# Kernel optimization log

Measured on AMD Instinct MI355X. Metric: run time of the kernel, lower is better.

## Reference

```python
import jax, jax.numpy as jnp
import numpy as np

N, E = 50000, 800000
D, H, C, ED = 128, 8, 16, 32  # in_channels, heads, head_dim, edge_dim
EPS = 1e-5

def _ln(x, g, b):
    mu = jnp.mean(x, axis=-1, keepdims=True)
    var = jnp.mean((x - mu) ** 2, axis=-1, keepdims=True)
    return (x - mu) * jax.lax.rsqrt(var + EPS) * g + b

def setup_inputs() -> dict:
    key = jax.random.key(0)
    ks = jax.random.split(key, 20)
    s = 0.05
    inp = {
        'x': jax.random.normal(ks[0], (N, D), jnp.float32),
        'edge_index': jax.random.randint(ks[1], (2, E), 0, N, jnp.int64),
        'edge_attr': jax.random.normal(ks[2], (E, ED), jnp.float32),
        'Wq': jax.random.normal(ks[3], (D, H * C)) * s,
        'bq': jnp.zeros((H * C,)),
        'Wk': jax.random.normal(ks[4], (D, H * C)) * s,
        'bk': jnp.zeros((H * C,)),
        'Wv': jax.random.normal(ks[5], (D, H * C)) * s,
        'bv': jnp.zeros((H * C,)),
        'We': jax.random.normal(ks[6], (ED, H * C)) * s,
        'Wskip': jax.random.normal(ks[7], (D, H * C)) * s,
        'bskip': jnp.zeros((H * C,)),
        'ln1_g': jnp.ones((D,)), 'ln1_b': jnp.zeros((D,)),
        'W1': jax.random.normal(ks[8], (D, 4 * D)) * s,
        'b1': jnp.zeros((4 * D,)),
        'W2': jax.random.normal(ks[9], (4 * D, D)) * s,
        'b2': jnp.zeros((D,)),
        'ln2_g': jnp.ones((D,)), 'ln2_b': jnp.zeros((D,)),
    }
    return inp

def reference(x, edge_index, edge_attr, Wq, bq, Wk, bk, Wv, bv, We, Wskip, bskip,
              ln1_g, ln1_b, W1, b1, W2, b2, ln2_g, ln2_b):
    src, dst = edge_index[0], edge_index[1]
    # node-level projections, then gather per-edge  [N,H,C] -> [E,H,C]
    q = (x @ Wq + bq).reshape(N, H, C)
    k = (x @ Wk + bk).reshape(N, H, C)
    v = (x @ Wv + bv).reshape(N, H, C)
    e = (edge_attr @ We).reshape(E, H, C)
    k_e = k[src] + e
    alpha = jnp.sum(q[dst] * k_e, axis=-1) / jnp.sqrt(jnp.float32(C))  # [E,H]
    # segment softmax over destination nodes
    m = jax.ops.segment_max(alpha, dst, num_segments=N)               # [N,H]
    p = jnp.exp(alpha - m[dst])
    denom = jax.ops.segment_sum(p, dst, num_segments=N)
    a = p / (denom[dst] + 1e-16)
    out_e = (v[src] + e) * a[..., None]                               # [E,H,C]
    attn = jax.ops.segment_sum(out_e, dst, num_segments=N).reshape(N, H * C)
    attn = attn + x @ Wskip + bskip  # root/skip connection
    # transformer block: residual + LN + FFN + LN (dropout = identity, eval)
    h = _ln(x + attn, ln1_g, ln1_b)
    ffn = jax.nn.relu(h @ W1 + b1) @ W2 + b2
    return _ln(h + ffn, ln2_g, ln2_b)
```

## Files before the change

kernel.cpp:

```cpp
#include <hip/hip_runtime.h>
#include <hip/hip_bf16.h>

using bf16 = __hip_bfloat16;
typedef __attribute__((ext_vector_type(8))) short short8;
typedef __attribute__((ext_vector_type(4))) float floatx4;

#define NN 50000
#define EE 800000
#define DD 128
#define HH 8
#define CC 16
#define EDD 32
#define DF 512

__device__ __forceinline__ float b2f(bf16 v) { return __bfloat162float(v); }
__device__ __forceinline__ float bs2f(short s) {
    bf16 h = *reinterpret_cast<bf16*>(&s);
    return __bfloat162float(h);
}
__device__ __forceinline__ float bu2f(unsigned short s) {
    unsigned int u = ((unsigned int)s) << 16;
    return *reinterpret_cast<float*>(&u);
}
__device__ __forceinline__ short f2bs(float v) {
    bf16 h = __float2bfloat16(v);
    return *reinterpret_cast<short*>(&h);
}

__global__ void k_detect(const int* __restrict__ ei, int* __restrict__ flag)
{
    if (threadIdx.x == 0 && blockIdx.x == 0) {
        int all0 = 1;
        for (int i = 0; i < 16; ++i) all0 &= (ei[2 * i + 1] == 0);
        flag[0] = all0;
    }
}

__device__ __forceinline__ int load_src(const int* ei, int is64, int i)
{
    int s = is64 ? ei[2 * i] : ei[i];
    return (s < 0) ? 0 : (s >= NN ? NN - 1 : s);
}
__device__ __forceinline__ int load_dst(const int* ei, int is64, int i)
{
    int d = is64 ? ei[2 * EE + 2 * i] : ei[EE + i];
    return (d < 0) ? 0 : (d >= NN ? NN - 1 : d);
}

__global__ void k_packall(const float* __restrict__ Wq, const float* __restrict__ Wk,
                          const float* __restrict__ Wv, const float* __restrict__ Wsk,
                          const float* __restrict__ W1, const float* __restrict__ W2,
                          const float* __restrict__ We,
                          bf16* __restrict__ wqp, bf16* __restrict__ wkp,
                          bf16* __restrict__ wvp, bf16* __restrict__ wskp,
                          bf16* __restrict__ w1p, bf16* __restrict__ w2p,
                          bf16* __restrict__ wep)
{
    int idx = blockIdx.x * 256 + threadIdx.x;
    const float* W; bf16* out; int ksteps, N, local;
    if (idx < 65536) {
        int wsel = idx >> 14; local = idx & 16383;
        W   = (wsel == 0) ? Wq  : (wsel == 1) ? Wk  : (wsel == 2) ? Wv  : Wsk;
        out = (wsel == 0) ? wqp : (wsel == 1) ? wkp : (wsel == 2) ? wvp : wskp;
        ksteps = 4; N = 128;
    } else if (idx < 131072) { local = idx - 65536;  W = W1; out = w1p; ksteps = 4;  N = 512; }
    else if (idx < 196608)   { local = idx - 131072; W = W2; out = w2p; ksteps = 16; N = 128; }
    else if (idx < 200704)   { local = idx - 196608; W = We; out = wep; ksteps = 1;  N = 128; }
    else return;
    int j = local & 7, lane = (local >> 3) & 63, rest = local >> 9;
    int kstep = rest % ksteps, ntile = rest / ksteps;
    int quad = lane >> 4, m = lane & 15;
    int k = kstep * 32 + quad * 8 + j;
    int n = ntile * 16 + m;
    out[local] = __float2bfloat16(W[(size_t)k * N + n]);
}

__global__ __launch_bounds__(256) void k_proj(
    const float* __restrict__ x,
    const bf16* __restrict__ wqp, const bf16* __restrict__ wkp,
    const bf16* __restrict__ wvp, const bf16* __restrict__ wskp,
    const float* __restrict__ bq, const float* __restrict__ bk,
    const float* __restrict__ bv, const float* __restrict__ bsk,
    bf16* __restrict__ qb, bf16* __restrict__ kb, bf16* __restrict__ vb,
    bf16* __restrict__ skipb)
{
    __shared__ __align__(16) short xs[32][136];
    __shared__ __align__(16) short os[32][520];
    const int t = threadIdx.x;
    const int wave = t >> 6, lane = t & 63;
    const int quad = lane >> 4, m = lane & 15;
    const int n0 = blockIdx.x * 32;

    for (int idx = t; idx < 32 * 32; idx += 256) {
        int row = idx >> 5, g = idx & 31;
        int node = n0 + row;
        float4 xv = {0.f, 0.f, 0.f, 0.f};
        if (node < NN) xv = *reinterpret_cast<const float4*>(&x[(size_t)node * 128 + g * 4]);
        short4 s4;
        s4.x = f2bs(xv.x); s4.y = f2bs(xv.y); s4.z = f2bs(xv.z); s4.w = f2bs(xv.w);
        *reinterpret_cast<short4*>(&xs[row][g * 4]) = s4;
    }
    __syncthreads();

    const bf16* Wp = (wave == 0) ? wqp : (wave == 1) ? wkp : (wave == 2) ? wvp : wskp;
    const float* bias = (wave == 0) ? bq : (wave == 1) ? bk : (wave == 2) ? bv : bsk;

    floatx4 acc[2][8];
#pragma unroll
    for (int mt = 0; mt < 2; ++mt)
#pragma unroll
        for (int nt = 0; nt < 8; ++nt) acc[mt][nt] = (floatx4){0.f, 0.f, 0.f, 0.f};

#pragma unroll
    for (int kstep = 0; kstep < 4; ++kstep) {
        short8 af0 = *reinterpret_cast<const short8*>(&xs[m][kstep * 32 + quad * 8]);
        short8 af1 = *reinterpret_cast<const short8*>(&xs[16 + m][kstep * 32 + quad * 8]);
#pragma unroll
        for (int nt = 0; nt < 8; ++nt) {
            short8 bf = *reinterpret_cast<const short8*>(
                reinterpret_cast<const short*>(Wp) + ((nt * 4 + kstep) * 64 + lane) * 8);
            acc[0][nt] = __builtin_amdgcn_mfma_f32_16x16x32_bf16(af0, bf, acc[0][nt], 0, 0, 0);
            acc[1][nt] = __builtin_amdgcn_mfma_f32_16x16x32_bf16(af1, bf, acc[1][nt], 0, 0, 0);
        }
    }
#pragma unroll
    for (int nt = 0; nt < 8; ++nt) {
        float bs = bias[nt * 16 + m];
#pragma unroll
        for (int mt = 0; mt < 2; ++mt)
#pragma unroll
            for (int r = 0; r < 4; ++r)
                os[mt * 16 + quad * 4 + r][wave * 128 + nt * 16 + m] = f2bs(acc[mt][nt][r] + bs);
    }
    __syncthreads();
    for (int idx = t; idx < 32 * 64; idx += 256) {
        int row = idx >> 6, g = idx & 63;
        int node = n0 + row;
        if (node >= NN) continue;
        int col0 = g * 8;
        bf16* dst = (col0 < 128) ? qb : (col0 < 256) ? kb : (col0 < 384) ? vb : skipb;
        *reinterpret_cast<float4*>(&dst[(size_t)node * 128 + (col0 & 127)]) =
            *reinterpret_cast<const float4*>(&os[row][col0]);
    }
}

__global__ void k_hist(const int* __restrict__ ei, const int* __restrict__ flag,
                       int* __restrict__ deg)
{
    int i = blockIdx.x * 256 + threadIdx.x;
    if (i >= EE) return;
    atomicAdd(&deg[load_dst(ei, flag[0], i)], 1);
}

__global__ __launch_bounds__(1024) void k_scan(const int* __restrict__ deg,
                                               int* __restrict__ rowstart)
{
    __shared__ int s[1024];
    const int t = threadIdx.x;
    const int CH = 49;
    int base = t * CH;
    int sum = 0;
    for (int i = 0; i < CH; i++) {
        int idx = base + i;
        if (idx < NN) sum += deg[idx];
    }
    s[t] = sum;
    __syncthreads();
    int own = sum;
    for (int off = 1; off < 1024; off <<= 1) {
        int v = (t >= off) ? s[t - off] : 0;
        __syncthreads();
        s[t] += v;
        __syncthreads();
    }
    int run = s[t] - own;
    for (int i = 0; i < CH; i++) {
        int idx = base + i;
        if (idx < NN) {
            rowstart[idx] = run;
            run += deg[idx];
        }
    }
    if (t == 0) rowstart[NN] = EE;
}

__global__ void k_scatter(const int* __restrict__ ei, const int* __restrict__ flag,
                          const int* __restrict__ rowstart,
                          int* __restrict__ cursor, int* __restrict__ srcs,
                          int* __restrict__ eids)
{
    int i = blockIdx.x * 256 + threadIdx.x;
    if (i >= EE) return;
    int is64 = flag[0];
    int d = load_dst(ei, is64, i);
    int pos = rowstart[d] + atomicAdd(&cursor[d], 1);
    srcs[pos] = load_src(ei, is64, i);
    eids[pos] = i;
}

__global__ __launch_bounds__(128) void k_attn(
    const float* __restrict__ x, const float* __restrict__ edge_attr,
    const bf16* __restrict__ wep,
    const bf16* __restrict__ qb, const bf16* __restrict__ kb,
    const bf16* __restrict__ vb, const bf16* __restrict__ skipb,
    const int* __restrict__ rowstart, const int* __restrict__ srcs,
    const int* __restrict__ eids,
    const float* __restrict__ ln1g, const float* __restrict__ ln1b,
    bf16* __restrict__ hb)
{
    __shared__ __align__(16) short es[16][136];
    __shared__ int ss[16];
    __shared__ float r1[2], r2[2];
    const int n = blockIdx.x;
    const int t = threadIdx.x;
    const int wave = t >> 6, lane = t & 63;
    const int quad = lane >> 4, m = lane & 15;

    short8 Bf[4];
#pragma unroll
    for (int ntl = 0; ntl < 4; ++ntl) {
        int nt = wave * 4 + ntl;
        Bf[ntl] = *reinterpret_cast<const short8*>(
            reinterpret_cast<const short*>(wep) + (nt * 64 + lane) * 8);
    }
    float q_t = b2f(qb[n * 128 + t]);
    const int eoff = rowstart[n], eend = rowstart[n + 1];
    const unsigned short* kbu = reinterpret_cast<const unsigned short*>(kb);
    const unsigned short* vbu = reinterpret_cast<const unsigned short*>(vb);
    float l = 0.f, acc = 0.f;

    for (int p0 = eoff; p0 < eend; p0 += 16) {
        int pos = p0 + m;
        int pc = (pos < eend) ? pos : eoff;
        int eid = eids[pc];
        const float* arow = edge_attr + (size_t)eid * 32 + quad * 8;
        float4 a0 = *reinterpret_cast<const float4*>(arow);
        float4 a1 = *reinterpret_cast<const float4*>(arow + 4);
        short8 Af;
        Af[0] = f2bs(a0.x); Af[1] = f2bs(a0.y); Af[2] = f2bs(a0.z); Af[3] = f2bs(a0.w);
        Af[4] = f2bs(a1.x); Af[5] = f2bs(a1.y); Af[6] = f2bs(a1.z); Af[7] = f2bs(a1.w);
        if (t < 16) ss[t] = srcs[(p0 + t < eend) ? p0 + t : eoff];
#pragma unroll
        for (int ntl = 0; ntl < 4; ++ntl) {
            floatx4 C = {0.f, 0.f, 0.f, 0.f};
            C = __builtin_amdgcn_mfma_f32_16x16x32_bf16(Af, Bf[ntl], C, 0, 0, 0);
            int col = (wave * 4 + ntl) * 16 + m;
#pragma unroll
            for (int r = 0; r < 4; ++r)
                es[quad * 4 + r][col] = f2bs(C[r]);
        }
        __syncthreads();
        int cnt = eend - p0; if (cnt > 16) cnt = 16;
        unsigned short kr[16], vr[16];
#pragma unroll
        for (int j = 0; j < 16; ++j) {
            size_t o = (size_t)ss[j] * 128 + t;
            kr[j] = kbu[o];
            vr[j] = vbu[o];
        }
#pragma unroll
        for (int j = 0; j < 16; ++j) {
            float e = bs2f(es[j][t]);
            float pr = q_t * (bu2f(kr[j]) + e);
            pr += __shfl_xor(pr, 1);
            pr += __shfl_xor(pr, 2);
            pr += __shfl_xor(pr, 4);
            pr += __shfl_xor(pr, 8);
            float w = (j < cnt) ? __expf(pr * 0.25f) : 0.f;
            l += w;
            acc = fmaf(bu2f(vr[j]) + e, w, acc);
        }
        __syncthreads();
    }
    float attn = acc / (l + 1e-16f);
    float pre = x[n * 128 + t] + attn + b2f(skipb[n * 128 + t]);
    float s1 = pre, s2 = pre * pre;
#pragma unroll
    for (int off = 1; off < 64; off <<= 1) {
        s1 += __shfl_xor(s1, off);
        s2 += __shfl_xor(s2, off);
    }
    const int wid = t >> 6;
    if (lane == 0) { r1[wid] = s1; r2[wid] = s2; }
    __syncthreads();
    float mu = (r1[0] + r1[1]) * (1.f / 128.f);
    float ms = (r2[0] + r2[1]) * (1.f / 128.f);
    float var = ms - mu * mu;
    float inv = rsqrtf(var + 1e-5f);
    float h = (pre - mu) * inv * ln1g[t] + ln1b[t];
    hb[n * 128 + t] = __float2bfloat16(h);
}

__global__ __launch_bounds__(256) void k_ffn(
    const bf16* __restrict__ hb,
    const bf16* __restrict__ w1p, const float* __restrict__ b1,
    const bf16* __restrict__ w2p, const float* __restrict__ b2,
    const float* __restrict__ ln2g, const float* __restrict__ ln2b,
    float* __restrict__ out)
{
    __shared__ __align__(16) short hs[32][136];
    __shared__ __align__(16) short t1s[32][520];
    float* fs = reinterpret_cast<float*>(&t1s[0][0]);
    const int t = threadIdx.x;
    const int wave = t >> 6, lane = t & 63;
    const int quad = lane >> 4, m = lane & 15;
    const int n0 = blockIdx.x * 32;

    for (int idx = t; idx < 32 * 16; idx += 256) {
        int row = idx >> 4, g = idx & 15;
        int node = n0 + row;
        if (node < NN) {
            *reinterpret_cast<float4*>(&hs[row][g * 8]) =
                *reinterpret_cast<const float4*>(&hb[(size_t)node * 128 + g * 8]);
        } else {
            float4 z = {0.f, 0.f, 0.f, 0.f};
            *reinterpret_cast<float4*>(&hs[row][g * 8]) = z;
        }
    }
    __syncthreads();

    floatx4 acc1[2][8];
#pragma unroll
    for (int mt = 0; mt < 2; ++mt)
#pragma unroll
        for (int nt = 0; nt < 8; ++nt) acc1[mt][nt] = (floatx4){0.f, 0.f, 0.f, 0.f};
#pragma unroll
    for (int kstep = 0; kstep < 4; ++kstep) {
        short8 af0 = *reinterpret_cast<const short8*>(&hs[m][kstep * 32 + quad * 8]);
        short8 af1 = *reinterpret_cast<const short8*>(&hs[16 + m][kstep * 32 + quad * 8]);
#pragma unroll
        for (int nt = 0; nt < 8; ++nt) {
            short8 bf = *reinterpret_cast<const short8*>(
                reinterpret_cast<const short*>(w1p) + (((wave * 8 + nt) * 4 + kstep) * 64 + lane) * 8);
            acc1[0][nt] = __builtin_amdgcn_mfma_f32_16x16x32_bf16(af0, bf, acc1[0][nt], 0, 0, 0);
            acc1[1][nt] = __builtin_amdgcn_mfma_f32_16x16x32_bf16(af1, bf, acc1[1][nt], 0, 0, 0);
        }
    }
#pragma unroll
    for (int nt = 0; nt < 8; ++nt) {
        float bs = b1[wave * 128 + nt * 16 + m];
#pragma unroll
        for (int mt = 0; mt < 2; ++mt)
#pragma unroll
            for (int r = 0; r < 4; ++r)
                t1s[mt * 16 + quad * 4 + r][wave * 128 + nt * 16 + m] =
                    f2bs(fmaxf(acc1[mt][nt][r] + bs, 0.f));
    }
    __syncthreads();

    floatx4 acc2[2][2];
#pragma unroll
    for (int mt = 0; mt < 2; ++mt)
#pragma unroll
        for (int nt = 0; nt < 2; ++nt) acc2[mt][nt] = (floatx4){0.f, 0.f, 0.f, 0.f};
#pragma unroll
    for (int kstep = 0; kstep < 16; ++kstep) {
        short8 af0 = *reinterpret_cast<const short8*>(&t1s[m][kstep * 32 + quad * 8]);
        short8 af1 = *reinterpret_cast<const short8*>(&t1s[16 + m][kstep * 32 + quad * 8]);
#pragma unroll
        for (int nt = 0; nt < 2; ++nt) {
            short8 bf = *reinterpret_cast<const short8*>(
                reinterpret_cast<const short*>(w2p) + (((wave * 2 + nt) * 16 + kstep) * 64 + lane) * 8);
            acc2[0][nt] = __builtin_amdgcn_mfma_f32_16x16x32_bf16(af0, bf, acc2[0][nt], 0, 0, 0);
            acc2[1][nt] = __builtin_amdgcn_mfma_f32_16x16x32_bf16(af1, bf, acc2[1][nt], 0, 0, 0);
        }
    }
    __syncthreads();
#pragma unroll
    for (int nt = 0; nt < 2; ++nt) {
        int col = (wave * 2 + nt) * 16 + m;
        float bs = b2[col];
#pragma unroll
        for (int mt = 0; mt < 2; ++mt)
#pragma unroll
            for (int r = 0; r < 4; ++r)
                fs[(mt * 16 + quad * 4 + r) * 132 + col] = acc2[mt][nt][r] + bs;
    }
    __syncthreads();

    for (int rr = 0; rr < 8; ++rr) {
        int row = wave * 8 + rr;
        int node = n0 + row;
        float p0 = bs2f(hs[row][lane]) + fs[row * 132 + lane];
        float p1 = bs2f(hs[row][lane + 64]) + fs[row * 132 + lane + 64];
        float s1 = p0 + p1, s2 = p0 * p0 + p1 * p1;
#pragma unroll
        for (int off = 1; off < 64; off <<= 1) {
            s1 += __shfl_xor(s1, off);
            s2 += __shfl_xor(s2, off);
        }
        float mu = s1 * (1.f / 128.f);
        float var = s2 * (1.f / 128.f) - mu * mu;
        float inv = rsqrtf(var + 1e-5f);
        if (node < NN) {
            out[(size_t)node * 128 + lane] = (p0 - mu) * inv * ln2g[lane] + ln2b[lane];
            out[(size_t)node * 128 + lane + 64] = (p1 - mu) * inv * ln2g[lane + 64] + ln2b[lane + 64];
        }
    }
}

extern "C" void kernel_launch(void* const* d_in, const int* in_sizes, int n_in,
                              void* d_out, int out_size, void* d_ws, size_t ws_size,
                              hipStream_t stream)
{
    const float* x    = (const float*)d_in[0];
    const int*   ei   = (const int*)d_in[1];
    const float* ea   = (const float*)d_in[2];
    const float* Wq   = (const float*)d_in[3];
    const float* bq   = (const float*)d_in[4];
    const float* Wk   = (const float*)d_in[5];
    const float* bk   = (const float*)d_in[6];
    const float* Wv   = (const float*)d_in[7];
    const float* bv   = (const float*)d_in[8];
    const float* We   = (const float*)d_in[9];
    const float* Wsk  = (const float*)d_in[10];
    const float* bsk  = (const float*)d_in[11];
    const float* ln1g = (const float*)d_in[12];
    const float* ln1b = (const float*)d_in[13];
    const float* W1   = (const float*)d_in[14];
    const float* b1   = (const float*)d_in[15];
    const float* W2   = (const float*)d_in[16];
    const float* b2   = (const float*)d_in[17];
    const float* ln2g = (const float*)d_in[18];
    const float* ln2b = (const float*)d_in[19];

    char* ws = (char*)d_ws;
    size_t off = 0;
    auto alloc = [&](size_t bytes) -> void* {
        void* p = ws + off;
        off += (bytes + 255) & ~(size_t)255;
        return p;
    };
    int*   flag     = (int*)alloc(256);
    int*   deg      = (int*)alloc((size_t)NN * 4);
    int*   cursor   = (int*)alloc((size_t)NN * 4);
    int*   rowstart = (int*)alloc((size_t)(NN + 1) * 4);
    int*   srcs     = (int*)alloc((size_t)EE * 4);
    int*   eids     = (int*)alloc((size_t)EE * 4);
    bf16*  qb       = (bf16*)alloc((size_t)NN * 128 * 2);
    bf16*  kb       = (bf16*)alloc((size_t)NN * 128 * 2);
    bf16*  vb       = (bf16*)alloc((size_t)NN * 128 * 2);
    bf16*  skipb    = (bf16*)alloc((size_t)NN * 128 * 2);
    bf16*  hb       = (bf16*)alloc((size_t)NN * 128 * 2);
    bf16*  wqp      = (bf16*)alloc((size_t)16384 * 2);
    bf16*  wkp      = (bf16*)alloc((size_t)16384 * 2);
    bf16*  wvp      = (bf16*)alloc((size_t)16384 * 2);
    bf16*  wskp     = (bf16*)alloc((size_t)16384 * 2);
    bf16*  w1p      = (bf16*)alloc((size_t)65536 * 2);
    bf16*  w2p      = (bf16*)alloc((size_t)65536 * 2);
    bf16*  wep      = (bf16*)alloc((size_t)4096 * 2);

    hipMemsetAsync(deg, 0, (size_t)NN * 4, stream);
    hipMemsetAsync(cursor, 0, (size_t)NN * 4, stream);

    k_detect<<<1, 64, 0, stream>>>(ei, flag);
    k_packall<<<(200704 + 255) / 256, 256, 0, stream>>>(
        Wq, Wk, Wv, Wsk, W1, W2, We, wqp, wkp, wvp, wskp, w1p, w2p, wep);
    k_hist<<<(EE + 255) / 256, 256, 0, stream>>>(ei, flag, deg);
    k_proj<<<(NN + 31) / 32, 256, 0, stream>>>(x, wqp, wkp, wvp, wskp,
                                               bq, bk, bv, bsk, qb, kb, vb, skipb);
    k_scan<<<1, 1024, 0, stream>>>(deg, rowstart);
    k_scatter<<<(EE + 255) / 256, 256, 0, stream>>>(ei, flag, rowstart, cursor, srcs, eids);
    k_attn<<<NN, 128, 0, stream>>>(x, ea, wep, qb, kb, vb, skipb,
                                   rowstart, srcs, eids, ln1g, ln1b, hb);
    k_ffn<<<(NN + 31) / 32, 256, 0, stream>>>(hb, w1p, b1, w2p, b2, ln2g, ln2b, (float*)d_out);
}
```

Before: 630.1 us.

## Interleave K/V per node, pack src/eid pairs, and map one node per wave in attention

The projection kernel now writes K and V interleaved as bf16 pairs, so one 8-byte load per lane fetches two channels of both K and V for a gathered source node. The scatter kernel writes (src, eid) as a single int2, which removes a separate index array read. The attention kernel processes one destination node per wave, four per block, with each lane handling two channels. This replaces block-wide syncthreads with wave barriers, drops one shuffle step, and stages We in LDS. The gathers for all 16 edges are issued before the MFMA, which raises per-lane register use and LDS footprint.

Measured after the change: 548.9 us. 1.15x faster.

```diff
diff --git a/kernel.cpp b/kernel.cpp
--- a/kernel.cpp
+++ b/kernel.cpp
@@ -81,7 +81,7 @@
     const bf16* __restrict__ wvp, const bf16* __restrict__ wskp,
     const float* __restrict__ bq, const float* __restrict__ bk,
     const float* __restrict__ bv, const float* __restrict__ bsk,
-    bf16* __restrict__ qb, bf16* __restrict__ kb, bf16* __restrict__ vb,
+    bf16* __restrict__ qb, unsigned int* __restrict__ kvb,
     bf16* __restrict__ skipb)
 {
     __shared__ __align__(16) short xs[32][136];
@@ -134,13 +134,19 @@
     }
     __syncthreads();
     for (int idx = t; idx < 32 * 64; idx += 256) {
-        int row = idx >> 6, g = idx & 63;
+        int row = idx >> 6, c = idx & 63;
         int node = n0 + row;
         if (node >= NN) continue;
-        int col0 = g * 8;
-        bf16* dst = (col0 < 128) ? qb : (col0 < 256) ? kb : (col0 < 384) ? vb : skipb;
-        *reinterpret_cast<float4*>(&dst[(size_t)node * 128 + (col0 & 127)]) =
-            *reinterpret_cast<const float4*>(&os[row][col0]);
+        unsigned int qu  = *reinterpret_cast<const unsigned int*>(&os[row][2 * c]);
+        unsigned int ku  = *reinterpret_cast<const unsigned int*>(&os[row][128 + 2 * c]);
+        unsigned int vu  = *reinterpret_cast<const unsigned int*>(&os[row][256 + 2 * c]);
+        unsigned int sku = *reinterpret_cast<const unsigned int*>(&os[row][384 + 2 * c]);
+        reinterpret_cast<unsigned int*>(qb)[(size_t)node * 64 + c] = qu;
+        reinterpret_cast<unsigned int*>(skipb)[(size_t)node * 64 + c] = sku;
+        uint2 kv;
+        kv.x = (ku & 0xffffu) | (vu << 16);
+        kv.y = (ku >> 16) | (vu & 0xffff0000u);
+        reinterpret_cast<uint2*>(kvb)[(size_t)node * 64 + c] = kv;
     }
 }
 
@@ -186,109 +192,121 @@
 
 __global__ void k_scatter(const int* __restrict__ ei, const int* __restrict__ flag,
                           const int* __restrict__ rowstart,
-                          int* __restrict__ cursor, int* __restrict__ srcs,
-                          int* __restrict__ eids)
+                          int* __restrict__ cursor, int2* __restrict__ srcid)
 {
     int i = blockIdx.x * 256 + threadIdx.x;
     if (i >= EE) return;
     int is64 = flag[0];
     int d = load_dst(ei, is64, i);
     int pos = rowstart[d] + atomicAdd(&cursor[d], 1);
-    srcs[pos] = load_src(ei, is64, i);
-    eids[pos] = i;
-}
-
-__global__ __launch_bounds__(128) void k_attn(
+    srcid[pos] = make_int2(load_src(ei, is64, i), i);
+}
+
+__global__ __launch_bounds__(256) void k_attn(
     const float* __restrict__ x, const float* __restrict__ edge_attr,
     const bf16* __restrict__ wep,
-    const bf16* __restrict__ qb, const bf16* __restrict__ kb,
-    const bf16* __restrict__ vb, const bf16* __restrict__ skipb,
-    const int* __restrict__ rowstart, const int* __restrict__ srcs,
-    const int* __restrict__ eids,
+    const bf16* __restrict__ qb, const unsigned int* __restrict__ kvb,
+    const bf16* __restrict__ skipb,
+    const int* __restrict__ rowstart, const int2* __restrict__ srcid,
     const float* __restrict__ ln1g, const float* __restrict__ ln1b,
     bf16* __restrict__ hb)
 {
-    __shared__ __align__(16) short es[16][136];
-    __shared__ int ss[16];
-    __shared__ float r1[2], r2[2];
-    const int n = blockIdx.x;
+    __shared__ __align__(16) short es[4][16][136];
+    __shared__ __align__(16) short wes[4096];
     const int t = threadIdx.x;
     const int wave = t >> 6, lane = t & 63;
     const int quad = lane >> 4, m = lane & 15;
-
-    short8 Bf[4];
-#pragma unroll
-    for (int ntl = 0; ntl < 4; ++ntl) {
-        int nt = wave * 4 + ntl;
-        Bf[ntl] = *reinterpret_cast<const short8*>(
-            reinterpret_cast<const short*>(wep) + (nt * 64 + lane) * 8);
-    }
-    float q_t = b2f(qb[n * 128 + t]);
+    const int n = blockIdx.x * 4 + wave;
+
+    for (int idx = t; idx < 512; idx += 256)
+        *reinterpret_cast<short8*>(&wes[idx * 8]) =
+            *reinterpret_cast<const short8*>(reinterpret_cast<const short*>(wep) + idx * 8);
+    __syncthreads();
+
+    short (*esw)[136] = es[wave];
+
+    unsigned int qp = reinterpret_cast<const unsigned int*>(qb)[(size_t)n * 64 + lane];
+    float q0 = bu2f((unsigned short)(qp & 0xffffu));
+    float q1 = bu2f((unsigned short)(qp >> 16));
+
     const int eoff = rowstart[n], eend = rowstart[n + 1];
-    const unsigned short* kbu = reinterpret_cast<const unsigned short*>(kb);
-    const unsigned short* vbu = reinterpret_cast<const unsigned short*>(vb);
-    float l = 0.f, acc = 0.f;
+    float lsum = 0.f, acc0 = 0.f, acc1 = 0.f;
 
     for (int p0 = eoff; p0 < eend; p0 += 16) {
         int pos = p0 + m;
         int pc = (pos < eend) ? pos : eoff;
-        int eid = eids[pc];
-        const float* arow = edge_attr + (size_t)eid * 32 + quad * 8;
+        int2 se = srcid[pc];
+
+        const float* arow = edge_attr + (size_t)se.y * 32 + quad * 8;
         float4 a0 = *reinterpret_cast<const float4*>(arow);
         float4 a1 = *reinterpret_cast<const float4*>(arow + 4);
+
+        uint2 kvr[16];
+#pragma unroll
+        for (int j = 0; j < 16; ++j) {
+            int sj = __builtin_amdgcn_readlane(se.x, j);
+            kvr[j] = reinterpret_cast<const uint2*>(kvb + (size_t)(unsigned)sj * 128)[lane];
+        }
+
         short8 Af;
         Af[0] = f2bs(a0.x); Af[1] = f2bs(a0.y); Af[2] = f2bs(a0.z); Af[3] = f2bs(a0.w);
         Af[4] = f2bs(a1.x); Af[5] = f2bs(a1.y); Af[6] = f2bs(a1.z); Af[7] = f2bs(a1.w);
-        if (t < 16) ss[t] = srcs[(p0 + t < eend) ? p0 + t : eoff];
-#pragma unroll
-        for (int ntl = 0; ntl < 4; ++ntl) {
+#pragma unroll
+        for (int nt = 0; nt < 8; ++nt) {
+            short8 Bf = *reinterpret_cast<const short8*>(&wes[(nt * 64 + lane) * 8]);
             floatx4 C = {0.f, 0.f, 0.f, 0.f};
-            C = __builtin_amdgcn_mfma_f32_16x16x32_bf16(Af, Bf[ntl], C, 0, 0, 0);
-            int col = (wave * 4 + ntl) * 16 + m;
+            C = __builtin_amdgcn_mfma_f32_16x16x32_bf16(Af, Bf, C, 0, 0, 0);
+            int col = nt * 16 + m;
 #pragma unroll
             for (int r = 0; r < 4; ++r)
-                es[quad * 4 + r][col] = f2bs(C[r]);
-        }
-        __syncthreads();
+                esw[quad * 4 + r][col] = f2bs(C[r]);
+        }
+        __builtin_amdgcn_wave_barrier();
+
         int cnt = eend - p0; if (cnt > 16) cnt = 16;
-        unsigned short kr[16], vr[16];
 #pragma unroll
         for (int j = 0; j < 16; ++j) {
-            size_t o = (size_t)ss[j] * 128 + t;
-            kr[j] = kbu[o];
-            vr[j] = vbu[o];
-        }
-#pragma unroll
-        for (int j = 0; j < 16; ++j) {
-            float e = bs2f(es[j][t]);
-            float pr = q_t * (bu2f(kr[j]) + e);
+            unsigned int eu = *reinterpret_cast<const unsigned int*>(&esw[j][2 * lane]);
+            float e0 = bu2f((unsigned short)(eu & 0xffffu));
+            float e1 = bu2f((unsigned short)(eu >> 16));
+            float k0 = bu2f((unsigned short)(kvr[j].x & 0xffffu));
+            float v0 = bu2f((unsigned short)(kvr[j].x >> 16));
+            float k1 = bu2f((unsigned short)(kvr[j].y & 0xffffu));
+            float v1 = bu2f((unsigned short)(kvr[j].y >> 16));
+            float pr = fmaf(k1 + e1, q1, (k0 + e0) * q0);
             pr += __shfl_xor(pr, 1);
             pr += __shfl_xor(pr, 2);
             pr += __shfl_xor(pr, 4);
-            pr += __shfl_xor(pr, 8);
             float w = (j < cnt) ? __expf(pr * 0.25f) : 0.f;
-            l += w;
-            acc = fmaf(bu2f(vr[j]) + e, w, acc);
-        }
-        __syncthreads();
-    }
-    float attn = acc / (l + 1e-16f);
-    float pre = x[n * 128 + t] + attn + b2f(skipb[n * 128 + t]);
-    float s1 = pre, s2 = pre * pre;
+            lsum += w;
+            acc0 = fmaf(v0 + e0, w, acc0);
+            acc1 = fmaf(v1 + e1, w, acc1);
+        }
+        __builtin_amdgcn_wave_barrier();
+    }
+
+    float rden = 1.f / (lsum + 1e-16f);
+    float attn0 = acc0 * rden, attn1 = acc1 * rden;
+    float2 xv = *reinterpret_cast<const float2*>(x + (size_t)n * 128 + 2 * lane);
+    unsigned int skp = reinterpret_cast<const unsigned int*>(skipb)[(size_t)n * 64 + lane];
+    float pre0 = xv.x + attn0 + bu2f((unsigned short)(skp & 0xffffu));
+    float pre1 = xv.y + attn1 + bu2f((unsigned short)(skp >> 16));
+    float s1 = pre0 + pre1, s2 = pre0 * pre0 + pre1 * pre1;
 #pragma unroll
     for (int off = 1; off < 64; off <<= 1) {
         s1 += __shfl_xor(s1, off);
         s2 += __shfl_xor(s2, off);
     }
-    const int wid = t >> 6;
-    if (lane == 0) { r1[wid] = s1; r2[wid] = s2; }
-    __syncthreads();
-    float mu = (r1[0] + r1[1]) * (1.f / 128.f);
-    float ms = (r2[0] + r2[1]) * (1.f / 128.f);
-    float var = ms - mu * mu;
+    float mu = s1 * (1.f / 128.f);
+    float var = s2 * (1.f / 128.f) - mu * mu;
     float inv = rsqrtf(var + 1e-5f);
-    float h = (pre - mu) * inv * ln1g[t] + ln1b[t];
-    hb[n * 128 + t] = __float2bfloat16(h);
+    float2 g  = *reinterpret_cast<const float2*>(ln1g + 2 * lane);
+    float2 bb = *reinterpret_cast<const float2*>(ln1b + 2 * lane);
+    float h0 = (pre0 - mu) * inv * g.x + bb.x;
+    float h1 = (pre1 - mu) * inv * g.y + bb.y;
+    unsigned int hu = (unsigned int)(unsigned short)f2bs(h0) |
+                      ((unsigned int)(unsigned short)f2bs(h1) << 16);
+    reinterpret_cast<unsigned int*>(hb)[(size_t)n * 64 + lane] = hu;
 }
 
 __global__ __launch_bounds__(256) void k_ffn(
@@ -435,11 +453,9 @@
     int*   deg      = (int*)alloc((size_t)NN * 4);
     int*   cursor   = (int*)alloc((size_t)NN * 4);
     int*   rowstart = (int*)alloc((size_t)(NN + 1) * 4);
-    int*   srcs     = (int*)alloc((size_t)EE * 4);
-    int*   eids     = (int*)alloc((size_t)EE * 4);
+    int2*  srcid    = (int2*)alloc((size_t)EE * 8);
     bf16*  qb       = (bf16*)alloc((size_t)NN * 128 * 2);
-    bf16*  kb       = (bf16*)alloc((size_t)NN * 128 * 2);
-    bf16*  vb       = (bf16*)alloc((size_t)NN * 128 * 2);
+    unsigned int* kvb = (unsigned int*)alloc((size_t)NN * 128 * 4);
     bf16*  skipb    = (bf16*)alloc((size_t)NN * 128 * 2);
     bf16*  hb       = (bf16*)alloc((size_t)NN * 128 * 2);
     bf16*  wqp      = (bf16*)alloc((size_t)16384 * 2);
@@ -458,10 +474,10 @@
         Wq, Wk, Wv, Wsk, W1, W2, We, wqp, wkp, wvp, wskp, w1p, w2p, wep);
     k_hist<<<(EE + 255) / 256, 256, 0, stream>>>(ei, flag, deg);
     k_proj<<<(NN + 31) / 32, 256, 0, stream>>>(x, wqp, wkp, wvp, wskp,
-                                               bq, bk, bv, bsk, qb, kb, vb, skipb);
+                                               bq, bk, bv, bsk, qb, kvb, skipb);
     k_scan<<<1, 1024, 0, stream>>>(deg, rowstart);
-    k_scatter<<<(EE + 255) / 256, 256, 0, stream>>>(ei, flag, rowstart, cursor, srcs, eids);
-    k_attn<<<NN, 128, 0, stream>>>(x, ea, wep, qb, kb, vb, skipb,
-                                   rowstart, srcs, eids, ln1g, ln1b, hb);
+    k_scatter<<<(EE + 255) / 256, 256, 0, stream>>>(ei, flag, rowstart, cursor, srcid);
+    k_attn<<<(NN + 3) / 4, 256, 0, stream>>>(x, ea, wep, qb, kvb, skipb,
+                                             rowstart, srcid, ln1g, ln1b, hb);
     k_ffn<<<(NN + 31) / 32, 256, 0, stream>>>(hb, w1p, b1, w2p, b2, ln2g, ln2b, (float*)d_out);
 }
```
